# Performance work log

Hardware: AMD Instinct MI355X
Metric: run time of the kernel (lower is better)

The kernel has to match this reference:

```python
import jax, jax.numpy as jnp
import numpy as np

MOMENTUM = 0.9


def setup_inputs() -> dict:
    key = jax.random.key(0)
    k1, k2, k3, k4 = jax.random.split(key, 4)
    B, D, C = 524288, 256, 1000
    x = jax.random.normal(k1, (B, D), dtype=jnp.float32)
    l = jax.random.randint(k2, (B,), 0, C, dtype=jnp.int64)
    center_img = jax.random.normal(k3, (C, D), dtype=jnp.float32)
    center_skt = jax.random.normal(k4, (C, D), dtype=jnp.float32)
    return {"x": x, "l": l, "center_img": center_img, "center_skt": center_skt}


def reference(x, l, center_img, center_skt):
    # Faithful vectorized version of CenterAlignment.forward (modality='img').
    # The per-sample Python scatter-add loop -> segment_sum over fixed num_classes;
    # torch.unique's data-dependent class set -> boolean 'present' mask.
    C = center_img.shape[0]
    counts = jax.ops.segment_sum(jnp.ones(x.shape[0], dtype=x.dtype), l, num_segments=C)  # [C]
    sums = jax.ops.segment_sum(x, l, num_segments=C)                                      # [C, D]
    present = counts > 0
    mean = sums / jnp.maximum(counts, 1.0)[:, None]  # per-class mean (safe div for absent classes)
    # momentum update + L2 renormalization, only for classes present in the batch
    upd = center_img * MOMENTUM + mean * (1.0 - MOMENTUM)
    upd = upd / jnp.linalg.norm(upd, axis=1, keepdims=True)
    new_img = jnp.where(present[:, None], upd, center_img)
    # align_loss with alpha=2: mean over present classes of ||c_img - c_skt||^2
    diff = new_img - center_skt
    sq = jnp.sum(diff * diff, axis=1)  # [C]
    n_present = jnp.maximum(jnp.sum(present.astype(x.dtype)), 1.0)
    loss = jnp.sum(jnp.where(present, sq, 0.0)) / n_present
    return loss
```

## Files before the change

### kernel.cpp

```cpp
#include <hip/hip_runtime.h>

#define CMAX    1000
#define CPAD    64
#define FIXS    1048576.0f
#define INVFIXS (1.0f / 1048576.0f)

__global__ __launch_bounds__(256) void hist_kernel(
    const int* __restrict__ l, int* __restrict__ tot, int B)
{
    __shared__ int h[CMAX];
    for (int i = threadIdx.x; i < CMAX; i += 256) h[i] = 0;
    __syncthreads();
    const int per  = (B + gridDim.x - 1) / gridDim.x;
    const int base = blockIdx.x * per;
    const int end  = min(B, base + per);
    for (int i = base + threadIdx.x; i < end; i += 256)
        atomicAdd(&h[l[i]], 1);
    __syncthreads();
    for (int i = threadIdx.x; i < CMAX; i += 256) {
        const int v = h[i];
        if (v) atomicAdd(&tot[i], v);
    }
}

__global__ __launch_bounds__(1024) void scan_kernel(
    const int* __restrict__ tot, int* __restrict__ cursor,
    int* __restrict__ cnt_i, int C)
{
    __shared__ int s[1024];
    const int t = threadIdx.x;
    const int v = (t < C) ? tot[t] : 0;
    s[t] = v;
    if (t < C) cnt_i[t] = v;
    for (int off = 1; off < 1024; off <<= 1) {
        __syncthreads();
        const int u = (t >= off) ? s[t - off] : 0;
        __syncthreads();
        s[t] += u;
    }
    __syncthreads();
    if (t < C) cursor[t * CPAD] = s[t] - v;
}

__global__ __launch_bounds__(256) void build_kernel(
    const int* __restrict__ l, int* __restrict__ cursor,
    int* __restrict__ perm, int* __restrict__ lsorted, int B)
{
    const int per  = (B + gridDim.x - 1) / gridDim.x;
    const int base = blockIdx.x * per;
    const int end  = min(B, base + per);
    for (int i = base + threadIdx.x; i < end; i += 256) {
        const int c   = l[i];
        const int pos = atomicAdd(&cursor[c * CPAD], 1);
        perm[pos]    = i;
        lsorted[pos] = c;
    }
}

#define SPAN 64
__global__ __launch_bounds__(256) void segsum_kernel(
    const float* __restrict__ x, const int* __restrict__ perm,
    const int* __restrict__ lsorted, int* __restrict__ sums_i, int B, int D)
{
    const int lane = threadIdx.x & 63;
    const int wid  = (int)((blockIdx.x * blockDim.x + threadIdx.x) >> 6);
    const int p0 = wid * SPAN;
    if (p0 >= B) return;
    const int p1 = min(B, p0 + SPAN);
    const int DV = D >> 2;
    const float4* __restrict__ x4 = (const float4*)x;

    int cur = lsorted[p0];
    int ax = 0, ay = 0, az = 0, aw = 0;

    int    c_n   = cur;
    int    idx_n = perm[p0];
    float4 v_n   = x4[(size_t)idx_n * DV + lane];

    for (int p = p0; p < p1; ++p) {
        const float4 v = v_n;
        const int    c = c_n;
        if (p + 1 < p1) {
            const int idx2 = perm[p + 1];
            c_n = lsorted[p + 1];
            v_n = x4[(size_t)idx2 * DV + lane];
        }
        if (c != cur) {
            int* dst = sums_i + (size_t)cur * D + (lane << 2);
            atomicAdd(dst + 0, ax);
            atomicAdd(dst + 1, ay);
            atomicAdd(dst + 2, az);
            atomicAdd(dst + 3, aw);
            ax = ay = az = aw = 0;
            cur = c;
        }
        ax += __float2int_rn(v.x * FIXS);
        ay += __float2int_rn(v.y * FIXS);
        az += __float2int_rn(v.z * FIXS);
        aw += __float2int_rn(v.w * FIXS);
    }
    int* dst = sums_i + (size_t)cur * D + (lane << 2);
    atomicAdd(dst + 0, ax);
    atomicAdd(dst + 1, ay);
    atomicAdd(dst + 2, az);
    atomicAdd(dst + 3, aw);
}

__device__ __forceinline__ float block_reduce_sum_256(float v, float* sbuf) {
    #pragma unroll
    for (int o = 32; o > 0; o >>= 1) v += __shfl_down(v, o, 64);
    __syncthreads();
    if ((threadIdx.x & 63) == 0) sbuf[threadIdx.x >> 6] = v;
    __syncthreads();
    return sbuf[0] + sbuf[1] + sbuf[2] + sbuf[3];
}

__global__ __launch_bounds__(256) void update_kernel(
    const int* __restrict__ sums_i, const int* __restrict__ cnt_i,
    const float* __restrict__ cimg, const float* __restrict__ cskt,
    float* __restrict__ sq_out, float* __restrict__ pres_out, int C, int D)
{
    __shared__ float sbuf[4];
    __shared__ float cshare;
    const int c = blockIdx.x;
    const int t = threadIdx.x;

    const float ssum = (float)sums_i[(size_t)c * D + t] * INVFIXS;
    if (t == 0) cshare = (float)cnt_i[c];
    __syncthreads();
    const float cnt = cshare;

    const bool present = cnt > 0.5f;
    const size_t idx = (size_t)c * D + t;
    const float ci = cimg[idx];
    const float cs = cskt[idx];
    const float mean = ssum / fmaxf(cnt, 1.f);
    const float upd = ci * 0.9f + mean * 0.1f;
    const float n2 = block_reduce_sum_256(upd * upd, sbuf);
    const float inv = 1.0f / sqrtf(n2);
    const float newv = present ? upd * inv : ci;
    const float df = newv - cs;
    const float sq = block_reduce_sum_256(df * df, sbuf);
    if (t == 0) {
        sq_out[c]   = present ? sq : 0.f;
        pres_out[c] = present ? 1.f : 0.f;
    }
}

__global__ __launch_bounds__(256) void finalize_kernel(
    const float* __restrict__ sq, const float* __restrict__ pres,
    float* __restrict__ out, int C)
{
    __shared__ float sbuf[4];
    float ls = 0.f, np = 0.f;
    for (int i = threadIdx.x; i < C; i += 256) {
        ls += sq[i];
        np += pres[i];
    }
    ls = block_reduce_sum_256(ls, sbuf);
    np = block_reduce_sum_256(np, sbuf);
    if (threadIdx.x == 0) out[0] = ls / fmaxf(np, 1.f);
}

extern "C" void kernel_launch(void* const* d_in, const int* in_sizes, int n_in,
                              void* d_out, int out_size, void* d_ws, size_t ws_size,
                              hipStream_t stream) {
    const float* x    = (const float*)d_in[0];
    const int*   l    = (const int*)d_in[1];
    const float* cimg = (const float*)d_in[2];
    const float* cskt = (const float*)d_in[3];

    const int B = in_sizes[1];
    const int D = in_sizes[0] / B;
    const int C = in_sizes[2] / D;

    int* ws_i     = (int*)d_ws;
    int* sums_i   = ws_i;
    int* tot      = sums_i + (size_t)C * D;
    int* cnt_i    = tot + C;
    int* cursor   = cnt_i + C;
    int* perm     = cursor + (size_t)C * CPAD;
    int* lsorted  = perm + B;
    float* sq     = (float*)(lsorted + B);
    float* pres   = sq + C;

    hipMemsetAsync(sums_i, 0, sizeof(int) * ((size_t)C * D + C), stream);

    hist_kernel<<<256, 256, 0, stream>>>(l, tot, B);
    scan_kernel<<<1, 1024, 0, stream>>>(tot, cursor, cnt_i, C);
    build_kernel<<<256, 256, 0, stream>>>(l, cursor, perm, lsorted, B);

    const int rowsPerBlock = 4 * SPAN;
    const int dblocks = (B + rowsPerBlock - 1) / rowsPerBlock;
    segsum_kernel<<<dblocks, 256, 0, stream>>>(x, perm, lsorted, sums_i, B, D);

    update_kernel<<<C, 256, 0, stream>>>(sums_i, cnt_i, cimg, cskt, sq, pres, C, D);
    finalize_kernel<<<1, 256, 0, stream>>>(sq, pres, (float*)d_out, C);
}
```

Measured before the change: 168.7 us.

## Build permutation with block-local histograms and find segments by binary search

The build kernel now computes a per-block shared-memory histogram, reserves one contiguous range per class with a single global atomic, and scatters indices using shared-memory atomics. This replaces one global atomic per element on padded cursors. The lsorted array is removed. Segsum instead binary-searches the class offsets for its start and walks the boundaries, and each wave loads its perm indices once and broadcasts them with shuffles. The risk is extra shared-memory atomics and a data-dependent boundary loop.

```diff
diff --git a/kernel.cpp b/kernel.cpp
--- a/kernel.cpp
+++ b/kernel.cpp
@@ -1,9 +1,11 @@
 #include <hip/hip_runtime.h>
 
 #define CMAX    1000
-#define CPAD    64
 #define FIXS    1048576.0f
 #define INVFIXS (1.0f / 1048576.0f)
+#define NB_HIST 256
+#define NB_BLD  128
+#define SPAN    64
 
 __global__ __launch_bounds__(256) void hist_kernel(
     const int* __restrict__ l, int* __restrict__ tot, int B)
@@ -24,8 +26,8 @@
 }
 
 __global__ __launch_bounds__(1024) void scan_kernel(
-    const int* __restrict__ tot, int* __restrict__ cursor,
-    int* __restrict__ cnt_i, int C)
+    const int* __restrict__ tot, int* __restrict__ offs,
+    int* __restrict__ gcur, int* __restrict__ cnt_i, int C, int B)
 {
     __shared__ int s[1024];
     const int t = threadIdx.x;
@@ -39,60 +41,84 @@
         s[t] += u;
     }
     __syncthreads();
-    if (t < C) cursor[t * CPAD] = s[t] - v;
-}
-
-__global__ __launch_bounds__(256) void build_kernel(
-    const int* __restrict__ l, int* __restrict__ cursor,
-    int* __restrict__ perm, int* __restrict__ lsorted, int B)
-{
+    if (t < C) {
+        const int e = s[t] - v;
+        offs[t] = e;
+        gcur[t] = e;
+    }
+    if (t == 0) offs[C] = B;
+}
+
+__global__ __launch_bounds__(1024) void build_kernel(
+    const int* __restrict__ l, int* __restrict__ gcur,
+    int* __restrict__ perm, int B)
+{
+    __shared__ int lhist[CMAX];
+    __shared__ int lbase[CMAX];
     const int per  = (B + gridDim.x - 1) / gridDim.x;
     const int base = blockIdx.x * per;
     const int end  = min(B, base + per);
-    for (int i = base + threadIdx.x; i < end; i += 256) {
-        const int c   = l[i];
-        const int pos = atomicAdd(&cursor[c * CPAD], 1);
-        perm[pos]    = i;
-        lsorted[pos] = c;
-    }
-}
-
-#define SPAN 64
+
+    for (int i = threadIdx.x; i < CMAX; i += 1024) lhist[i] = 0;
+    __syncthreads();
+    for (int i = base + threadIdx.x; i < end; i += 1024)
+        atomicAdd(&lhist[l[i]], 1);
+    __syncthreads();
+    for (int c = threadIdx.x; c < CMAX; c += 1024) {
+        const int n = lhist[c];
+        lbase[c] = n ? atomicAdd(&gcur[c], n) : 0;
+        lhist[c] = 0;
+    }
+    __syncthreads();
+    for (int i = base + threadIdx.x; i < end; i += 1024) {
+        const int c = l[i];
+        const int r = atomicAdd(&lhist[c], 1);
+        perm[lbase[c] + r] = i;
+    }
+}
+
 __global__ __launch_bounds__(256) void segsum_kernel(
     const float* __restrict__ x, const int* __restrict__ perm,
-    const int* __restrict__ lsorted, int* __restrict__ sums_i, int B, int D)
+    const int* __restrict__ offs, int* __restrict__ sums_i,
+    int B, int D, int C)
 {
     const int lane = threadIdx.x & 63;
     const int wid  = (int)((blockIdx.x * blockDim.x + threadIdx.x) >> 6);
     const int p0 = wid * SPAN;
     if (p0 >= B) return;
-    const int p1 = min(B, p0 + SPAN);
+    const int n  = min(SPAN, B - p0);
     const int DV = D >> 2;
     const float4* __restrict__ x4 = (const float4*)x;
 
-    int cur = lsorted[p0];
+    const int myidx = (p0 + lane < B) ? perm[p0 + lane] : 0;
+
+    int lo = 0, hi = C - 1;
+    while (lo < hi) {
+        const int mid = (lo + hi + 1) >> 1;
+        if (offs[mid] <= p0) lo = mid; else hi = mid - 1;
+    }
+    int cur = lo;
+    int nxt = offs[cur + 1];
+
     int ax = 0, ay = 0, az = 0, aw = 0;
-
-    int    c_n   = cur;
-    int    idx_n = perm[p0];
-    float4 v_n   = x4[(size_t)idx_n * DV + lane];
-
-    for (int p = p0; p < p1; ++p) {
-        const float4 v = v_n;
-        const int    c = c_n;
-        if (p + 1 < p1) {
-            const int idx2 = perm[p + 1];
-            c_n = lsorted[p + 1];
-            v_n = x4[(size_t)idx2 * DV + lane];
-        }
-        if (c != cur) {
-            int* dst = sums_i + (size_t)cur * D + (lane << 2);
-            atomicAdd(dst + 0, ax);
-            atomicAdd(dst + 1, ay);
-            atomicAdd(dst + 2, az);
-            atomicAdd(dst + 3, aw);
-            ax = ay = az = aw = 0;
-            cur = c;
+    float4 vnext = x4[(size_t)__shfl(myidx, 0, 64) * DV + lane];
+
+    for (int it = 0; it < n; ++it) {
+        const float4 v = vnext;
+        if (it + 1 < n)
+            vnext = x4[(size_t)__shfl(myidx, it + 1, 64) * DV + lane];
+        const int p = p0 + it;
+        while (p >= nxt) {
+            if (ax | ay | az | aw) {
+                int* dst = sums_i + (size_t)cur * D + (lane << 2);
+                atomicAdd(dst + 0, ax);
+                atomicAdd(dst + 1, ay);
+                atomicAdd(dst + 2, az);
+                atomicAdd(dst + 3, aw);
+                ax = ay = az = aw = 0;
+            }
+            ++cur;
+            nxt = offs[cur + 1];
         }
         ax += __float2int_rn(v.x * FIXS);
         ay += __float2int_rn(v.y * FIXS);
@@ -174,25 +200,24 @@
     const int D = in_sizes[0] / B;
     const int C = in_sizes[2] / D;
 
-    int* ws_i     = (int*)d_ws;
-    int* sums_i   = ws_i;
-    int* tot      = sums_i + (size_t)C * D;
-    int* cnt_i    = tot + C;
-    int* cursor   = cnt_i + C;
-    int* perm     = cursor + (size_t)C * CPAD;
-    int* lsorted  = perm + B;
-    float* sq     = (float*)(lsorted + B);
-    float* pres   = sq + C;
+    int* sums_i = (int*)d_ws;
+    int* tot    = sums_i + (size_t)C * D;
+    int* cnt_i  = tot + C;
+    int* offs   = cnt_i + C;
+    int* gcur   = offs + C + 1;
+    int* perm   = gcur + C;
+    float* sq   = (float*)(perm + B);
+    float* pres = sq + C;
 
     hipMemsetAsync(sums_i, 0, sizeof(int) * ((size_t)C * D + C), stream);
 
-    hist_kernel<<<256, 256, 0, stream>>>(l, tot, B);
-    scan_kernel<<<1, 1024, 0, stream>>>(tot, cursor, cnt_i, C);
-    build_kernel<<<256, 256, 0, stream>>>(l, cursor, perm, lsorted, B);
-
-    const int rowsPerBlock = 4 * SPAN;
-    const int dblocks = (B + rowsPerBlock - 1) / rowsPerBlock;
-    segsum_kernel<<<dblocks, 256, 0, stream>>>(x, perm, lsorted, sums_i, B, D);
+    hist_kernel<<<NB_HIST, 256, 0, stream>>>(l, tot, B);
+    scan_kernel<<<1, 1024, 0, stream>>>(tot, offs, gcur, cnt_i, C, B);
+    build_kernel<<<NB_BLD, 1024, 0, stream>>>(l, gcur, perm, B);
+
+    const int waves   = (B + SPAN - 1) / SPAN;
+    const int dblocks = (waves + 3) / 4;
+    segsum_kernel<<<dblocks, 256, 0, stream>>>(x, perm, offs, sums_i, B, D, C);
 
     update_kernel<<<C, 256, 0, stream>>>(sums_i, cnt_i, cimg, cskt, sq, pres, C, D);
     finalize_kernel<<<1, 256, 0, stream>>>(sq, pres, (float*)d_out, C);
```

Measured after the change: 140.1 us. 1.2x faster.
